# Optimization experiments

Measured on AMD Instinct MI355X. Metric: run time of the kernel, lower is better.

## Reference

```python
import jax, jax.numpy as jnp
import numpy as np

N, D, OUT, K = 100000, 256, 128, 10
N1, B = 40960, 4096


def setup_inputs() -> dict:
    key = jax.random.key(0)
    k1, k2, k3, k4, k5, k6, k7 = jax.random.split(key, 7)
    raw_features = jax.random.normal(k1, (N, D), dtype=jnp.float32)
    # xavier-ish init for SageLayer weights [out, 2*in]
    W1 = jax.random.normal(k2, (OUT, 2 * D), dtype=jnp.float32) * (2.0 / (OUT + 2 * D)) ** 0.5
    W2 = jax.random.normal(k3, (OUT, 2 * OUT), dtype=jnp.float32) * (2.0 / (OUT + 2 * OUT)) ** 0.5
    nodes1 = jax.random.randint(k4, (N1,), 0, N)              # layer-1 node ids into raw table
    neighs1 = jax.random.randint(k5, (N1, K), 0, N)           # sampled neighbors (ids into raw table)
    map2 = jax.random.randint(k6, (B,), 0, N1)                # self-index of batch nodes into layer-1 rows
    neighs2 = jax.random.randint(k7, (B, K), 0, N1)           # sampled neighbors (rows of layer-1 embs)
    return {"raw_features": raw_features, "W1": W1, "W2": W2,
            "nodes1": nodes1, "neighs1": neighs1, "map2": map2, "neighs2": neighs2}


def reference(raw_features, W1, W2, nodes1, neighs1, map2, neighs2):
    # Layer 1: mean-aggregate sampled neighbor features (= mask.div(num_neigh).mm(embed_matrix))
    agg1 = jnp.mean(raw_features[neighs1], axis=1)                      # [N1, D]
    self1 = raw_features[nodes1]                                        # [N1, D]
    h1 = jax.nn.relu(jnp.concatenate([self1, agg1], axis=1) @ W1.T)     # [N1, OUT]
    # Layer 2
    agg2 = jnp.mean(h1[neighs2], axis=1)                                # [B, OUT]
    self2 = h1[map2]                                                    # [B, OUT]
    h2 = jax.nn.relu(jnp.concatenate([self2, agg2], axis=1) @ W2.T)     # [B, OUT]
    return h2
```

## Files before the change

kernel.cpp:

```cpp
#include <hip/hip_runtime.h>
#include <hip/hip_bf16.h>

#define N_RAW  100000
#define DIM    256
#define OUTD   128
#define KN     10
#define N1N    40960
#define BATCH  4096

#define SNP    6252
#define NBP    512
#define SNQ    2560
#define NBQ    256

typedef __attribute__((ext_vector_type(8))) short bf16x8;
typedef __attribute__((ext_vector_type(4))) float f32x4;
typedef unsigned int u32;

static __device__ inline float b2f(short s) {
  unsigned u = ((unsigned)(unsigned short)s) << 16;
  return __builtin_bit_cast(float, u);
}
static __device__ inline short f2b(float f) {
  unsigned u = __builtin_bit_cast(unsigned, f);
  unsigned r = (u + 0x7fff + ((u >> 16) & 1)) >> 16;
  return (short)r;
}

__global__ void build_wc(const float* __restrict__ W1, const float* __restrict__ W2,
                         short* __restrict__ W1c, short* __restrict__ W2c) {
  int i = blockIdx.x * blockDim.x + threadIdx.x;
  {
    int j = i >> 8, k = i & 255;
    float v = (j < OUTD) ? W1[j * (2 * DIM) + k] : W1[(j - OUTD) * (2 * DIM) + DIM + k];
    W1c[j * 256 + k] = f2b(v);
  }
  if (i < 256 * 128) {
    int j = i >> 7, k = i & 127;
    float v = (j < OUTD) ? W2[j * (2 * OUTD) + k] : W2[(j - OUTD) * (2 * OUTD) + OUTD + k];
    W2c[j * 128 + k] = f2b(v);
  }
}

__launch_bounds__(256, 2)
__global__ void gemm_P(const float* __restrict__ raw, const short* __restrict__ W1c,
                       short* __restrict__ P) {
  const int tid  = threadIdx.x;
  const int wave = tid >> 6, lane = tid & 63;
  const int r16  = lane & 15, kg = lane >> 4;
  const int col0 = wave * 64;

  bf16x8 B[4][8];
#pragma unroll
  for (int n = 0; n < 4; ++n)
#pragma unroll
    for (int ks = 0; ks < 8; ++ks)
      B[n][ks] = *(const bf16x8*)(W1c + (size_t)(col0 + n * 16 + r16) * 256 + ks * 32 + kg * 8);

  int s = blockIdx.x;
  float4 af[16];
  {
    int r = s * 16 + r16; if (r > N_RAW - 1) r = N_RAW - 1;
    const float* x = raw + (size_t)r * DIM + kg * 8;
#pragma unroll
    for (int ks = 0; ks < 8; ++ks) {
      af[2 * ks]     = *(const float4*)(x + ks * 32);
      af[2 * ks + 1] = *(const float4*)(x + ks * 32 + 4);
    }
  }

  for (; s < SNP; s += NBP) {
    bf16x8 ab[8];
#pragma unroll
    for (int ks = 0; ks < 8; ++ks) {
      float4 lo = af[2 * ks], hi = af[2 * ks + 1];
      bf16x8 t;
      t[0] = f2b(lo.x); t[1] = f2b(lo.y); t[2] = f2b(lo.z); t[3] = f2b(lo.w);
      t[4] = f2b(hi.x); t[5] = f2b(hi.y); t[6] = f2b(hi.z); t[7] = f2b(hi.w);
      ab[ks] = t;
    }
    {
      int sn = s + NBP; if (sn >= SNP) sn = s;
      int r = sn * 16 + r16; if (r > N_RAW - 1) r = N_RAW - 1;
      const float* x = raw + (size_t)r * DIM + kg * 8;
#pragma unroll
      for (int ks = 0; ks < 8; ++ks) {
        af[2 * ks]     = *(const float4*)(x + ks * 32);
        af[2 * ks + 1] = *(const float4*)(x + ks * 32 + 4);
      }
    }

    f32x4 acc[4];
#pragma unroll
    for (int n = 0; n < 4; ++n) acc[n] = (f32x4){0.f, 0.f, 0.f, 0.f};
#pragma unroll
    for (int ks = 0; ks < 8; ++ks)
#pragma unroll
      for (int n = 0; n < 4; ++n)
        acc[n] = __builtin_amdgcn_mfma_f32_16x16x32_bf16(ab[ks], B[n][ks], acc[n], 0, 0, 0);

    int rbase = s * 16 + kg * 4;
#pragma unroll
    for (int n = 0; n < 4; ++n)
#pragma unroll
      for (int j = 0; j < 4; ++j) {
        int r = rbase + j;
        if (r < N_RAW) P[(size_t)r * 256 + (col0 + n * 16 + r16)] = f2b(acc[n][j]);
      }
  }
}

__launch_bounds__(256, 3)
__global__ void gemm_Q(const short* __restrict__ h1, const short* __restrict__ W2c,
                       short* __restrict__ Q) {
  const int tid  = threadIdx.x;
  const int wave = tid >> 6, lane = tid & 63;
  const int r16  = lane & 15, kg = lane >> 4;
  const int col0 = wave * 64;

  bf16x8 B[4][4];
#pragma unroll
  for (int n = 0; n < 4; ++n)
#pragma unroll
    for (int ks = 0; ks < 4; ++ks)
      B[n][ks] = *(const bf16x8*)(W2c + (size_t)(col0 + n * 16 + r16) * 128 + ks * 32 + kg * 8);

  int s = blockIdx.x;
  bf16x8 acur[4];
  {
    const short* x = h1 + (size_t)(s * 16 + r16) * OUTD + kg * 8;
#pragma unroll
    for (int ks = 0; ks < 4; ++ks) acur[ks] = *(const bf16x8*)(x + ks * 32);
  }

  for (; s < SNQ; s += NBQ) {
    bf16x8 anxt[4];
    {
      int sn = s + NBQ; if (sn >= SNQ) sn = s;
      const short* x = h1 + (size_t)(sn * 16 + r16) * OUTD + kg * 8;
#pragma unroll
      for (int ks = 0; ks < 4; ++ks) anxt[ks] = *(const bf16x8*)(x + ks * 32);
    }

    f32x4 acc[4];
#pragma unroll
    for (int n = 0; n < 4; ++n) acc[n] = (f32x4){0.f, 0.f, 0.f, 0.f};
#pragma unroll
    for (int ks = 0; ks < 4; ++ks)
#pragma unroll
      for (int n = 0; n < 4; ++n)
        acc[n] = __builtin_amdgcn_mfma_f32_16x16x32_bf16(acur[ks], B[n][ks], acc[n], 0, 0, 0);

    int rbase = s * 16 + kg * 4;
#pragma unroll
    for (int n = 0; n < 4; ++n)
#pragma unroll
      for (int j = 0; j < 4; ++j)
        Q[(size_t)(rbase + j) * 256 + (col0 + n * 16 + r16)] = f2b(acc[n][j]);

#pragma unroll
    for (int ks = 0; ks < 4; ++ks) acur[ks] = anxt[ks];
  }
}

__global__ void gather1(const short* __restrict__ P, const int* __restrict__ nodes1,
                        const int* __restrict__ neighs1, short* __restrict__ h1) {
  int g = threadIdx.x >> 4, t = threadIdx.x & 15;
  int row = blockIdx.x * 16 + g;
  int sn = nodes1[row];
  bf16x8 sv = *(const bf16x8*)(P + (size_t)sn * 256 + t * 8);
  float acc[8];
#pragma unroll
  for (int e = 0; e < 8; ++e) acc[e] = 0.f;
#pragma unroll
  for (int k = 0; k < KN; ++k) {
    int nn = neighs1[row * KN + k];
    bf16x8 nv = *(const bf16x8*)(P + (size_t)nn * 256 + 128 + t * 8);
#pragma unroll
    for (int e = 0; e < 8; ++e) acc[e] += b2f(nv[e]);
  }
  bf16x8 o;
#pragma unroll
  for (int e = 0; e < 8; ++e) o[e] = f2b(fmaxf(b2f(sv[e]) + 0.1f * acc[e], 0.f));
  *(bf16x8*)(h1 + (size_t)row * OUTD + t * 8) = o;
}

__global__ void gather2(const short* __restrict__ Q, const int* __restrict__ map2,
                        const int* __restrict__ neighs2, float* __restrict__ out) {
  int g = threadIdx.x >> 4, t = threadIdx.x & 15;
  int row = blockIdx.x * 16 + g;
  int sn = map2[row];
  bf16x8 sv = *(const bf16x8*)(Q + (size_t)sn * 256 + t * 8);
  float acc[8];
#pragma unroll
  for (int e = 0; e < 8; ++e) acc[e] = 0.f;
#pragma unroll
  for (int k = 0; k < KN; ++k) {
    int nn = neighs2[row * KN + k];
    bf16x8 nv = *(const bf16x8*)(Q + (size_t)nn * 256 + 128 + t * 8);
#pragma unroll
    for (int e = 0; e < 8; ++e) acc[e] += b2f(nv[e]);
  }
  float* orow = out + (size_t)row * OUTD + t * 8;
  float4 o0, o1;
  o0.x = fmaxf(b2f(sv[0]) + 0.1f * acc[0], 0.f);
  o0.y = fmaxf(b2f(sv[1]) + 0.1f * acc[1], 0.f);
  o0.z = fmaxf(b2f(sv[2]) + 0.1f * acc[2], 0.f);
  o0.w = fmaxf(b2f(sv[3]) + 0.1f * acc[3], 0.f);
  o1.x = fmaxf(b2f(sv[4]) + 0.1f * acc[4], 0.f);
  o1.y = fmaxf(b2f(sv[5]) + 0.1f * acc[5], 0.f);
  o1.z = fmaxf(b2f(sv[6]) + 0.1f * acc[6], 0.f);
  o1.w = fmaxf(b2f(sv[7]) + 0.1f * acc[7], 0.f);
  *(float4*)orow = o0;
  *(float4*)(orow + 4) = o1;
}

extern "C" void kernel_launch(void* const* d_in, const int* in_sizes, int n_in,
                              void* d_out, int out_size, void* d_ws, size_t ws_size,
                              hipStream_t stream) {
  const float* raw     = (const float*)d_in[0];
  const float* W1      = (const float*)d_in[1];
  const float* W2      = (const float*)d_in[2];
  const int*   nodes1  = (const int*)d_in[3];
  const int*   neighs1 = (const int*)d_in[4];
  const int*   map2    = (const int*)d_in[5];
  const int*   neighs2 = (const int*)d_in[6];
  float* out = (float*)d_out;

  char* ws = (char*)d_ws;
  short* W1c = (short*)(ws);
  short* W2c = (short*)(ws + 131072);
  short* P   = (short*)(ws + 196608);
  short* Q   = (short*)(ws + 196608);
  short* h1  = (short*)(ws + 51396608);

  build_wc<<<256, 256, 0, stream>>>(W1, W2, W1c, W2c);
  gemm_P<<<NBP, 256, 0, stream>>>(raw, W1c, P);
  gather1<<<N1N / 16, 256, 0, stream>>>(P, nodes1, neighs1, h1);
  gemm_Q<<<NBQ, 256, 0, stream>>>(h1, W2c, Q);
  gather2<<<BATCH / 16, 256, 0, stream>>>(Q, map2, neighs2, out);
}
```

Before: 111.9 us.

## Split GEMM columns across eight waves and use packed bf16 conversion

Both projection GEMMs now use 512-thread blocks, and each of the eight waves covers 32 output columns instead of 64. This halves the per-wave B fragments and accumulators, and the grid sizes are retuned (fewer blocks for gemm_P, more for gemm_Q). The fp32-to-bf16 conversion of raw features now uses the hardware v_cvt_pk_bf16_f32 instruction instead of software rounding. Each A row is now loaded by twice as many waves, which adds redundant global traffic on a memory-bound phase. Fewer blocks for gemm_P could also reduce latency hiding.

```diff
diff --git a/kernel.cpp b/kernel.cpp
--- a/kernel.cpp
+++ b/kernel.cpp
@@ -9,12 +9,13 @@
 #define BATCH  4096
 
 #define SNP    6252
-#define NBP    512
+#define NBP    256
 #define SNQ    2560
-#define NBQ    256
+#define NBQ    512
 
 typedef __attribute__((ext_vector_type(8))) short bf16x8;
 typedef __attribute__((ext_vector_type(4))) float f32x4;
+typedef __attribute__((ext_vector_type(4))) unsigned int u32x4;
 typedef unsigned int u32;
 
 static __device__ inline float b2f(short s) {
@@ -25,6 +26,11 @@
   unsigned u = __builtin_bit_cast(unsigned, f);
   unsigned r = (u + 0x7fff + ((u >> 16) & 1)) >> 16;
   return (short)r;
+}
+static __device__ inline u32 cvtpk(float lo, float hi) {
+  u32 r;
+  asm("v_cvt_pk_bf16_f32 %0, %1, %2" : "=v"(r) : "v"(lo), "v"(hi));
+  return r;
 }
 
 __global__ void build_wc(const float* __restrict__ W1, const float* __restrict__ W2,
@@ -42,17 +48,17 @@
   }
 }
 
-__launch_bounds__(256, 2)
-__global__ void gemm_P(const float* __restrict__ raw, const short* __restrict__ W1c,
-                       short* __restrict__ P) {
+__global__ __launch_bounds__(512) __attribute__((amdgpu_waves_per_eu(2, 2)))
+void gemm_P(const float* __restrict__ raw, const short* __restrict__ W1c,
+            short* __restrict__ P) {
   const int tid  = threadIdx.x;
   const int wave = tid >> 6, lane = tid & 63;
   const int r16  = lane & 15, kg = lane >> 4;
-  const int col0 = wave * 64;
-
-  bf16x8 B[4][8];
-#pragma unroll
-  for (int n = 0; n < 4; ++n)
+  const int col0 = wave * 32;
+
+  bf16x8 B[2][8];
+#pragma unroll
+  for (int n = 0; n < 2; ++n)
 #pragma unroll
     for (int ks = 0; ks < 8; ++ks)
       B[n][ks] = *(const bf16x8*)(W1c + (size_t)(col0 + n * 16 + r16) * 256 + ks * 32 + kg * 8);
@@ -74,10 +80,10 @@
 #pragma unroll
     for (int ks = 0; ks < 8; ++ks) {
       float4 lo = af[2 * ks], hi = af[2 * ks + 1];
-      bf16x8 t;
-      t[0] = f2b(lo.x); t[1] = f2b(lo.y); t[2] = f2b(lo.z); t[3] = f2b(lo.w);
-      t[4] = f2b(hi.x); t[5] = f2b(hi.y); t[6] = f2b(hi.z); t[7] = f2b(hi.w);
-      ab[ks] = t;
+      u32x4 t;
+      t.x = cvtpk(lo.x, lo.y); t.y = cvtpk(lo.z, lo.w);
+      t.z = cvtpk(hi.x, hi.y); t.w = cvtpk(hi.z, hi.w);
+      ab[ks] = __builtin_bit_cast(bf16x8, t);
     }
     {
       int sn = s + NBP; if (sn >= SNP) sn = s;
@@ -90,18 +96,18 @@
       }
     }
 
-    f32x4 acc[4];
-#pragma unroll
-    for (int n = 0; n < 4; ++n) acc[n] = (f32x4){0.f, 0.f, 0.f, 0.f};
-#pragma unroll
-    for (int ks = 0; ks < 8; ++ks)
-#pragma unroll
-      for (int n = 0; n < 4; ++n)
-        acc[n] = __builtin_amdgcn_mfma_f32_16x16x32_bf16(ab[ks], B[n][ks], acc[n], 0, 0, 0);
+    f32x4 acc[2];
+    acc[0] = (f32x4){0.f, 0.f, 0.f, 0.f};
+    acc[1] = (f32x4){0.f, 0.f, 0.f, 0.f};
+#pragma unroll
+    for (int ks = 0; ks < 8; ++ks) {
+      acc[0] = __builtin_amdgcn_mfma_f32_16x16x32_bf16(ab[ks], B[0][ks], acc[0], 0, 0, 0);
+      acc[1] = __builtin_amdgcn_mfma_f32_16x16x32_bf16(ab[ks], B[1][ks], acc[1], 0, 0, 0);
+    }
 
     int rbase = s * 16 + kg * 4;
 #pragma unroll
-    for (int n = 0; n < 4; ++n)
+    for (int n = 0; n < 2; ++n)
 #pragma unroll
       for (int j = 0; j < 4; ++j) {
         int r = rbase + j;
@@ -110,56 +116,56 @@
   }
 }
 
-__launch_bounds__(256, 3)
-__global__ void gemm_Q(const short* __restrict__ h1, const short* __restrict__ W2c,
-                       short* __restrict__ Q) {
+__global__ __launch_bounds__(512)
+void gemm_Q(const short* __restrict__ h1, const short* __restrict__ W2c,
+            short* __restrict__ Q) {
   const int tid  = threadIdx.x;
   const int wave = tid >> 6, lane = tid & 63;
   const int r16  = lane & 15, kg = lane >> 4;
-  const int col0 = wave * 64;
-
-  bf16x8 B[4][4];
-#pragma unroll
-  for (int n = 0; n < 4; ++n)
+  const int col0 = wave * 32;
+
+  bf16x8 B[2][4];
+#pragma unroll
+  for (int n = 0; n < 2; ++n)
 #pragma unroll
     for (int ks = 0; ks < 4; ++ks)
       B[n][ks] = *(const bf16x8*)(W2c + (size_t)(col0 + n * 16 + r16) * 128 + ks * 32 + kg * 8);
 
   int s = blockIdx.x;
-  bf16x8 acur[4];
+  bf16x8 a[4];
   {
     const short* x = h1 + (size_t)(s * 16 + r16) * OUTD + kg * 8;
 #pragma unroll
-    for (int ks = 0; ks < 4; ++ks) acur[ks] = *(const bf16x8*)(x + ks * 32);
+    for (int ks = 0; ks < 4; ++ks) a[ks] = *(const bf16x8*)(x + ks * 32);
   }
 
   for (; s < SNQ; s += NBQ) {
-    bf16x8 anxt[4];
+    bf16x8 an[4];
     {
       int sn = s + NBQ; if (sn >= SNQ) sn = s;
       const short* x = h1 + (size_t)(sn * 16 + r16) * OUTD + kg * 8;
 #pragma unroll
-      for (int ks = 0; ks < 4; ++ks) anxt[ks] = *(const bf16x8*)(x + ks * 32);
-    }
-
-    f32x4 acc[4];
-#pragma unroll
-    for (int n = 0; n < 4; ++n) acc[n] = (f32x4){0.f, 0.f, 0.f, 0.f};
-#pragma unroll
-    for (int ks = 0; ks < 4; ++ks)
-#pragma unroll
-      for (int n = 0; n < 4; ++n)
-        acc[n] = __builtin_amdgcn_mfma_f32_16x16x32_bf16(acur[ks], B[n][ks], acc[n], 0, 0, 0);
+      for (int ks = 0; ks < 4; ++ks) an[ks] = *(const bf16x8*)(x + ks * 32);
+    }
+
+    f32x4 acc[2];
+    acc[0] = (f32x4){0.f, 0.f, 0.f, 0.f};
+    acc[1] = (f32x4){0.f, 0.f, 0.f, 0.f};
+#pragma unroll
+    for (int ks = 0; ks < 4; ++ks) {
+      acc[0] = __builtin_amdgcn_mfma_f32_16x16x32_bf16(a[ks], B[0][ks], acc[0], 0, 0, 0);
+      acc[1] = __builtin_amdgcn_mfma_f32_16x16x32_bf16(a[ks], B[1][ks], acc[1], 0, 0, 0);
+    }
 
     int rbase = s * 16 + kg * 4;
 #pragma unroll
-    for (int n = 0; n < 4; ++n)
+    for (int n = 0; n < 2; ++n)
 #pragma unroll
       for (int j = 0; j < 4; ++j)
         Q[(size_t)(rbase + j) * 256 + (col0 + n * 16 + r16)] = f2b(acc[n][j]);
 
 #pragma unroll
-    for (int ks = 0; ks < 4; ++ks) acur[ks] = anxt[ks];
+    for (int ks = 0; ks < 4; ++ks) a[ks] = an[ks];
   }
 }
 
@@ -235,8 +241,8 @@
   short* h1  = (short*)(ws + 51396608);
 
   build_wc<<<256, 256, 0, stream>>>(W1, W2, W1c, W2c);
-  gemm_P<<<NBP, 256, 0, stream>>>(raw, W1c, P);
+  gemm_P<<<NBP, 512, 0, stream>>>(raw, W1c, P);
   gather1<<<N1N / 16, 256, 0, stream>>>(P, nodes1, neighs1, h1);
-  gemm_Q<<<NBQ, 256, 0, stream>>>(h1, W2c, Q);
+  gemm_Q<<<NBQ, 512, 0, stream>>>(h1, W2c, Q);
   gather2<<<BATCH / 16, 256, 0, stream>>>(Q, map2, neighs2, out);
 }
```

After: 159.2 us. 1.42x slower.
